# Kernel optimization log

Measured on AMD Instinct MI355X. Metric: run time of the kernel, lower is better.

## Reference

```python
import jax, jax.numpy as jnp
import numpy as np

D = 1024
H = 16
HD = D // H  # 64
LN_EPS = 1e-5


def _layernorm(x, w, b):
    m = jnp.mean(x, axis=-1, keepdims=True)
    v = jnp.mean(jnp.square(x - m), axis=-1, keepdims=True)
    return (x - m) * jax.lax.rsqrt(v + LN_EPS) * w + b


def _attention(x, w_qkv, b_qkv, w_proj, b_proj):
    # x: [B, S, D]. Block-diagonal mask == attention within each sequence,
    # so batched per-sequence attention is exactly equivalent to packed fmha.
    B, S, _ = x.shape
    qkv = x @ w_qkv + b_qkv                      # [B, S, 3D]
    q, k, v = jnp.split(qkv, 3, axis=-1)
    q = q.reshape(B, S, H, HD)
    k = k.reshape(B, S, H, HD)
    v = v.reshape(B, S, H, HD)
    scale = 1.0 / jnp.sqrt(jnp.asarray(HD, dtype=x.dtype))
    scores = jnp.einsum('bqhd,bkhd->bhqk', q, k) * scale  # [B, H, S, S]
    probs = jax.nn.softmax(scores, axis=-1)
    out = jnp.einsum('bhqk,bkhd->bqhd', probs, v).reshape(B, S, D)
    return out @ w_proj + b_proj


def _block(x, w_qkv, b_qkv, w_proj, b_proj, ln1_w, ln1_b,
           w_fc1, b_fc1, w_fc2, b_fc2, ln2_w, ln2_b, gamma1, gamma2):
    # x = x + ls1(attn(norm1(x)))
    x = x + gamma1 * _attention(_layernorm(x, ln1_w, ln1_b), w_qkv, b_qkv, w_proj, b_proj)
    # x = x + ls2(mlp(norm2(x)))
    h = _layernorm(x, ln2_w, ln2_b)
    h = jax.nn.gelu(h @ w_fc1 + b_fc1, approximate=False) @ w_fc2 + b_fc2
    return x + gamma2 * h


def setup_inputs() -> dict:
    key = jax.random.key(0)
    ks = jax.random.split(key, 8)
    s = 0.02
    return {
        'x1': jax.random.normal(ks[0], (8, 1024, D), jnp.float32),
        'x2': jax.random.normal(ks[1], (8, 512, D), jnp.float32),
        'w_qkv': jax.random.normal(ks[2], (D, 3 * D), jnp.float32) * s,
        'b_qkv': jnp.zeros((3 * D,), jnp.float32),
        'w_proj': jax.random.normal(ks[3], (D, D), jnp.float32) * s,
        'b_proj': jnp.zeros((D,), jnp.float32),
        'ln1_w': jnp.ones((D,), jnp.float32),
        'ln1_b': jnp.zeros((D,), jnp.float32),
        'ln2_w': jnp.ones((D,), jnp.float32),
        'ln2_b': jnp.zeros((D,), jnp.float32),
        'w_fc1': jax.random.normal(ks[4], (D, 4 * D), jnp.float32) * s,
        'b_fc1': jnp.zeros((4 * D,), jnp.float32),
        'w_fc2': jax.random.normal(ks[5], (4 * D, D), jnp.float32) * s,
        'b_fc2': jnp.zeros((D,), jnp.float32),
        'gamma1': jnp.full((D,), 1e-5, jnp.float32),  # LayerScale init_values
        'gamma2': jnp.full((D,), 1e-5, jnp.float32),
    }


def reference(x1, x2, w_qkv, b_qkv, w_proj, b_proj, ln1_w, ln1_b,
              ln2_w, ln2_b, w_fc1, b_fc1, w_fc2, b_fc2, gamma1, gamma2):
    params = (w_qkv, b_qkv, w_proj, b_proj, ln1_w, ln1_b,
              w_fc1, b_fc1, w_fc2, b_fc2, ln2_w, ln2_b, gamma1, gamma2)
    y1 = _block(x1, *params)
    y2 = _block(x2, *params)
    return (y1, y2)
```

## Files before the change

kernel.cpp:

```cpp
#include <hip/hip_runtime.h>
#include <cstddef>


typedef __bf16 b16x8 __attribute__((ext_vector_type(8)));
typedef float f32x4 __attribute__((ext_vector_type(4)));
typedef unsigned short u16x8 __attribute__((ext_vector_type(8)));
typedef unsigned short u16x4 __attribute__((ext_vector_type(4)));
typedef float f32x4v __attribute__((ext_vector_type(4)));

__device__ __forceinline__ unsigned short f2bf(float f) {
    unsigned int u = __builtin_bit_cast(unsigned int, f);
    return (unsigned short)((u + 0x7fffu + ((u >> 16) & 1u)) >> 16);
}
__device__ __forceinline__ unsigned short f2bf_trunc(float f) {
    return (unsigned short)(__builtin_bit_cast(unsigned int, f) >> 16);
}

__device__ __forceinline__ float exp2_f(float x) {
#if defined(__has_builtin)
#if __has_builtin(__builtin_amdgcn_exp2f)
    return __builtin_amdgcn_exp2f(x);
#else
    return exp2f(x);
#endif
#else
    return exp2f(x);
#endif
}

#define AS1C(p) ((const __attribute__((address_space(1))) void*)(p))
#define AS3(p)  ((__attribute__((address_space(3))) void*)(p))
#define FENCE() asm volatile("" ::: "memory")

__global__ __launch_bounds__(256) void wtrans_k(const float* __restrict__ in,
                                                unsigned short* __restrict__ out,
                                                int K, int N) {
    __shared__ float tile[32][33];
    int n0 = blockIdx.x << 5, k0 = blockIdx.y << 5;
    int tx = threadIdx.x & 31;
    int ty = threadIdx.x >> 5;
#pragma unroll
    for (int j = 0; j < 4; ++j)
        tile[ty + j * 8][tx] = in[(size_t)(k0 + ty + j * 8) * N + n0 + tx];
    __syncthreads();
#pragma unroll
    for (int j = 0; j < 4; ++j)
        out[(size_t)(n0 + ty + j * 8) * K + k0 + tx] = f2bf(tile[tx][ty + j * 8]);
}

__global__ __launch_bounds__(256) void vtrans_k(const unsigned short* __restrict__ qkv,
                                                unsigned short* __restrict__ vT) {
    __shared__ unsigned short tile[32][40];
    int tok0 = blockIdx.x << 5, c0 = blockIdx.y << 5;
    int tx = threadIdx.x & 31, ty = threadIdx.x >> 5;
#pragma unroll
    for (int j = 0; j < 4; ++j)
        tile[ty + j * 8][tx] = qkv[(size_t)(tok0 + ty + j * 8) * 3072 + 2048 + c0 + tx];
    __syncthreads();
#pragma unroll
    for (int j = 0; j < 4; ++j)
        vT[(size_t)(c0 + ty + j * 8) * 12288 + tok0 + tx] = tile[tx][ty + j * 8];
}

__global__ __launch_bounds__(256) void ln_k(const float* __restrict__ srcA,
                                            const float* __restrict__ srcB, int split,
                                            const float* __restrict__ w,
                                            const float* __restrict__ b,
                                            unsigned short* __restrict__ out) {
    int row = blockIdx.x;
    const float* src = (row < split) ? srcA + (size_t)row * 1024
                                     : srcB + (size_t)(row - split) * 1024;
    int t = threadIdx.x;
    f32x4v v = *(const f32x4v*)(src + t * 4);
    float s = v[0] + v[1] + v[2] + v[3];
    float s2 = v[0] * v[0] + v[1] * v[1] + v[2] * v[2] + v[3] * v[3];
#pragma unroll
    for (int off = 1; off < 64; off <<= 1) {
        s += __shfl_xor(s, off);
        s2 += __shfl_xor(s2, off);
    }
    __shared__ float red[8];
    int wv4 = t >> 6;
    if ((t & 63) == 0) { red[wv4 * 2] = s; red[wv4 * 2 + 1] = s2; }
    __syncthreads();
    s = red[0] + red[2] + red[4] + red[6];
    s2 = red[1] + red[3] + red[5] + red[7];
    float mean = s * (1.0f / 1024.0f);
    float var = s2 * (1.0f / 1024.0f) - mean * mean;
    float rstd = rsqrtf(var + 1e-5f);
    f32x4v wv = *(const f32x4v*)(w + t * 4);
    f32x4v bv = *(const f32x4v*)(b + t * 4);
    u16x4 ov;
#pragma unroll
    for (int j = 0; j < 4; ++j) ov[j] = f2bf((v[j] - mean) * rstd * wv[j] + bv[j]);
    *(u16x4*)(out + (size_t)row * 1024 + t * 4) = ov;
}

template <int BM, int K, int NN, int EPI>
__global__ __launch_bounds__(512, 1) void gemm3_k(
    const unsigned short* __restrict__ A, const unsigned short* __restrict__ BT,
    const float* __restrict__ bias, const float* __restrict__ scale,
    const float* __restrict__ rx1, const float* __restrict__ rx2,
    float* __restrict__ outf, unsigned short* __restrict__ outb) {
    constexpr int NT = K / 64;
    constexpr int ntn = NN >> 8;
    constexpr int GA = BM / 64;
    constexpr int NFR = BM / 32;
    constexpr int HALF = NFR / 2;
    constexpr int ABUF = BM * 128;
    constexpr int STRIDE = ABUF + 32768;
    __shared__ char lds[2 * STRIDE];
    const int t = threadIdx.x;
    const int lane = t & 63, w = t >> 6, lr = lane & 15, lg = lane >> 4;
    const int wm = w >> 2, wn = w & 3;
    const int nwg = gridDim.x;
    const int bid = blockIdx.x;
    const int swz = (bid & 7) * (nwg >> 3) + (bid >> 3);
    const int m0 = (swz / ntn) * BM;
    const int n0 = (swz % ntn) << 8;

    const int srow = t >> 3;
    const int scol = ((t & 7) ^ (srow & 7)) * 8;
    const unsigned short* ga = A + (size_t)(m0 + srow) * K + scol;
    const unsigned short* gb = BT + (size_t)(n0 + srow) * K + scol;

    f32x4 acc[NFR][4] = {};
    b16x8 af[HALF][2], b01[2][2], b23[2][2];

    auto ISSUE_A = [&](int tile, int g) {
        char* dst = lds + (tile & 1) * STRIDE + g * 8192 + t * 16;
        __builtin_amdgcn_global_load_lds(AS1C(ga + (size_t)(g * 64) * K + tile * 64),
                                         AS3(dst), 16, 0, 0);
    };
    auto ISSUE_B = [&](int tile, int g) {
        char* dst = lds + (tile & 1) * STRIDE + ABUF + g * 8192 + t * 16;
        __builtin_amdgcn_global_load_lds(AS1C(gb + (size_t)(g * 64) * K + tile * 64),
                                         AS3(dst), 16, 0, 0);
    };

    const int cs0 = (lg ^ (lr & 7)) * 16;
    const int cs1 = ((4 + lg) ^ (lr & 7)) * 16;

    auto RD_A = [&](const char* buf, int mg) {
#pragma unroll
        for (int mi = 0; mi < HALF; ++mi) {
            const char* p = buf + (wm * (BM / 2) + (mg + mi) * 16 + lr) * 128;
            af[mi][0] = *(const b16x8*)(p + cs0);
            af[mi][1] = *(const b16x8*)(p + cs1);
        }
    };
    auto RD_B = [&](const char* buf, b16x8 (*bf)[2], int ng) {
#pragma unroll
        for (int ni = 0; ni < 2; ++ni) {
            const char* p = buf + ABUF + (wn * 64 + (ng + ni) * 16 + lr) * 128;
            bf[ni][0] = *(const b16x8*)(p + cs0);
            bf[ni][1] = *(const b16x8*)(p + cs1);
        }
    };
    auto MM = [&](int mg, b16x8 (*bf)[2], int ng) {
        __builtin_amdgcn_s_setprio(1);
#pragma unroll
        for (int kk = 0; kk < 2; ++kk)
#pragma unroll
            for (int mi = 0; mi < HALF; ++mi)
#pragma unroll
                for (int ni = 0; ni < 2; ++ni)
                    acc[mg + mi][ng + ni] = __builtin_amdgcn_mfma_f32_16x16x32_bf16(
                        af[mi][kk], bf[ni][kk], acc[mg + mi][ng + ni], 0, 0, 0);
        __builtin_amdgcn_s_setprio(0);
    };
    auto WAIT_GA = [&]() {
        if constexpr (GA == 4) asm volatile("s_waitcnt vmcnt(4)" ::: "memory");
        else                   asm volatile("s_waitcnt vmcnt(3)" ::: "memory");
    };

#pragma unroll
    for (int g = 0; g < GA; ++g) ISSUE_A(0, g);
#pragma unroll
    for (int g = 0; g < 4; ++g) ISSUE_B(0, g);
#pragma unroll
    for (int g = 0; g < GA; ++g) ISSUE_A(1, g);
    WAIT_GA();
    __builtin_amdgcn_s_barrier();
    FENCE();

    for (int kt = 0; kt < NT; ++kt) {
        const char* buf = lds + (kt & 1) * STRIDE;
        RD_A(buf, 0); RD_B(buf, b01, 0);
        if (kt + 1 < NT) { ISSUE_B(kt + 1, 0); ISSUE_B(kt + 1, 1); }
        __builtin_amdgcn_s_barrier(); FENCE();
        MM(0, b01, 0);
        __builtin_amdgcn_s_barrier(); FENCE();
        RD_B(buf, b23, 2);
        if (kt + 1 < NT) { ISSUE_B(kt + 1, 2); ISSUE_B(kt + 1, 3); }
        __builtin_amdgcn_s_barrier(); FENCE();
        MM(0, b23, 2);
        __builtin_amdgcn_s_barrier(); FENCE();
        RD_A(buf, HALF);
        __builtin_amdgcn_s_barrier(); FENCE();
        MM(HALF, b23, 2);
        __builtin_amdgcn_s_barrier(); FENCE();
        if (kt + 2 < NT) {
#pragma unroll
            for (int g = 0; g < GA; ++g) ISSUE_A(kt + 2, g);
        }
        __builtin_amdgcn_s_barrier(); FENCE();
        MM(HALF, b01, 0);
        if (kt + 1 < NT) {
            if (kt + 2 < NT) WAIT_GA();
            else             asm volatile("s_waitcnt vmcnt(0)" ::: "memory");
            __builtin_amdgcn_s_barrier(); FENCE();
        }
    }

    if (EPI == 0 || EPI == 2) {
        __syncthreads();
        char* clb = lds;
        const int rl0 = wm * (BM / 2) + lg * 4;
        const int cl0 = wn * 64 + lr;
#pragma unroll
        for (int n = 0; n < 4; ++n) {
            const int col_l = cl0 + n * 16;
            const float bval = bias[n0 + col_l];
            const int colByte = col_l * 2;
            const int within = colByte & 15;
            const int chunk = colByte >> 4;
#pragma unroll
            for (int m = 0; m < NFR; ++m) {
#pragma unroll
                for (int r = 0; r < 4; ++r) {
                    float c = acc[m][n][r] + bval;
                    if (EPI == 2) {
                        float u = c * (c * c * 0.044715f + 1.0f) * 1.5957691216057308f;
                        c = c * __builtin_amdgcn_rcpf(1.0f + __expf(-u));
                    }
                    const int row_l = rl0 + m * 16 + r;
                    *(unsigned short*)(clb + row_l * 512 +
                                       (((chunk ^ (row_l & 7)) << 4) | within)) = f2bf(c);
                }
            }
        }
        __syncthreads();
#pragma unroll
        for (int it = 0; it < BM / 16; ++it) {
            int idx = it * 512 + t;
            int row = idx >> 5, ch = idx & 31;
            u16x8 v = *(const u16x8*)(clb + row * 512 + ((ch ^ (row & 7)) << 4));
            *(u16x8*)(outb + (size_t)(m0 + row) * NN + n0 + ch * 8) = v;
        }
    } else {
        const int rbase = m0 + wm * (BM / 2) + lg * 4;
        const int cbase = n0 + wn * 64 + lr;
#pragma unroll
        for (int n = 0; n < 4; ++n) {
            int col = cbase + n * 16;
            float bval = bias[col];
            float sval = scale[col];
#pragma unroll
            for (int m = 0; m < NFR; ++m) {
                int row = rbase + m * 16;
#pragma unroll
                for (int r = 0; r < 4; ++r) {
                    float c = acc[m][n][r] + bval;
                    size_t idx = (size_t)(row + r) * NN + col;
                    if (EPI == 1) {
                        float xv = (row + r < 8192) ? rx1[idx] : rx2[idx - (size_t)8192 * 1024];
                        outf[idx] = xv + sval * c;
                    } else {
                        outf[idx] += sval * c;
                    }
                }
            }
        }
    }
}

__global__ __launch_bounds__(512) void attn_k(const unsigned short* __restrict__ qkv,
                                              const unsigned short* __restrict__ vT,
                                              unsigned short* __restrict__ aout) {
    __shared__ char sK[2][8192];
    __shared__ char sV[2][8192];
    __shared__ unsigned short sP[8][16 * 72];
    const int xcd = blockIdx.x & 7;
    const int idx = blockIdx.x >> 3;
    int seq0, S, h, qt;
    if (idx < 128) {
        h = idx & 15; qt = idx >> 4; seq0 = xcd << 10; S = 1024;
    } else {
        int j = idx - 128;
        h = j & 15; qt = j >> 4; seq0 = 8192 + (xcd << 9); S = 512;
    }
    int t = threadIdx.x, lane = t & 63, w = t >> 6, lr = lane & 15, lg = lane >> 4;
    int tok0 = seq0 + qt * 128;
    const size_t hoff = (size_t)h * 64;

    const int srow = t >> 3;
    const int sc = ((t & 7) ^ (srow & 7)) * 8;
    const unsigned short* kg = qkv + (size_t)(seq0 + srow) * 3072 + 1024 + hoff + sc;
    const unsigned short* vg = vT + (size_t)(hoff + srow) * 12288 + seq0 + sc;

    b16x8 aq0, aq1;
    {
        const unsigned short* qb = qkv + (size_t)(tok0 + w * 16 + lr) * 3072 + hoff;
        aq0 = *(const b16x8*)(qb + lg * 8);
        aq1 = *(const b16x8*)(qb + 32 + lg * 8);
    }

    auto STAGE = [&](int kt) {
        int slot = kt & 1;
        __builtin_amdgcn_global_load_lds(AS1C(kg + (size_t)(kt << 6) * 3072),
                                         AS3(sK[slot] + t * 16), 16, 0, 0);
        __builtin_amdgcn_global_load_lds(AS1C(vg + (kt << 6)),
                                         AS3(sV[slot] + t * 16), 16, 0, 0);
    };

    const int swz0 = (lg ^ (lr & 7)) * 16;
    const int swz1 = ((4 + lg) ^ (lr & 7)) * 16;
    const float SC = 0.18033688f;

    float m_run[4] = {-1e30f, -1e30f, -1e30f, -1e30f};
    float l_run[4] = {0.f, 0.f, 0.f, 0.f};
    f32x4 o[4] = {};
    unsigned short* sPw = sP[w];
    const int nkv = S >> 6;

    auto QK = [&](int kt, f32x4 (&s)[4]) {
        const char* kb = sK[kt & 1];
#pragma unroll
        for (int n = 0; n < 4; ++n) {
            const char* kr = kb + (n * 16 + lr) * 128;
            b16x8 bk0 = *(const b16x8*)(kr + swz0);
            b16x8 bk1 = *(const b16x8*)(kr + swz1);
            f32x4 z = {};
            z = __builtin_amdgcn_mfma_f32_16x16x32_bf16(aq0, bk0, z, 0, 0, 0);
            z = __builtin_amdgcn_mfma_f32_16x16x32_bf16(aq1, bk1, z, 0, 0, 0);
            s[n] = z * SC;
        }
    };
    auto SM = [&](f32x4 (&s)[4], b16x8& a0, b16x8& a1) {
        float p[4][4];
#pragma unroll
        for (int r = 0; r < 4; ++r) {
            float tm = fmaxf(fmaxf(s[0][r], s[1][r]), fmaxf(s[2][r], s[3][r]));
            tm = fmaxf(tm, __shfl_xor(tm, 1));
            tm = fmaxf(tm, __shfl_xor(tm, 2));
            tm = fmaxf(tm, __shfl_xor(tm, 4));
            tm = fmaxf(tm, __shfl_xor(tm, 8));
            float mn = fmaxf(m_run[r], tm);
            float alpha = exp2_f(m_run[r] - mn);
            m_run[r] = mn;
            float rs = 0.f;
#pragma unroll
            for (int n = 0; n < 4; ++n) {
                float pv = exp2_f(s[n][r] - mn);
                p[n][r] = pv;
                rs += pv;
            }
            rs += __shfl_xor(rs, 1);
            rs += __shfl_xor(rs, 2);
            rs += __shfl_xor(rs, 4);
            rs += __shfl_xor(rs, 8);
            l_run[r] = l_run[r] * alpha + rs;
#pragma unroll
            for (int n = 0; n < 4; ++n) o[n][r] *= alpha;
        }
#pragma unroll
        for (int r = 0; r < 4; ++r)
#pragma unroll
            for (int n = 0; n < 4; ++n)
                sPw[(lg * 4 + r) * 72 + n * 16 + lr] = f2bf_trunc(p[n][r]);
        a0 = *(const b16x8*)(&sPw[lr * 72 + lg * 8]);
        a1 = *(const b16x8*)(&sPw[lr * 72 + 32 + lg * 8]);
    };

    STAGE(0);
    if (nkv > 1) STAGE(1);
    asm volatile("s_waitcnt vmcnt(0)" ::: "memory");
    __builtin_amdgcn_s_barrier();
    FENCE();
    f32x4 s0[4];
    QK(0, s0);
    b16x8 ap0, ap1;
    SM(s0, ap0, ap1);

    for (int kt = 0; kt < nkv; ++kt) {
        const char* vb = sV[kt & 1];
        b16x8 bv0[4], bv1[4];
#pragma unroll
        for (int n = 0; n < 4; ++n) {
            const char* vr = vb + (n * 16 + lr) * 128;
            bv0[n] = *(const b16x8*)(vr + swz0);
            bv1[n] = *(const b16x8*)(vr + swz1);
        }
        f32x4 s2[4];
        if (kt + 1 < nkv) QK(kt + 1, s2);
        asm volatile("s_waitcnt lgkmcnt(0)" ::: "memory");
        __builtin_amdgcn_s_barrier();
        FENCE();
        if (kt + 2 < nkv) STAGE(kt + 2);
#pragma unroll
        for (int n = 0; n < 4; ++n) {
            o[n] = __builtin_amdgcn_mfma_f32_16x16x32_bf16(ap0, bv0[n], o[n], 0, 0, 0);
            o[n] = __builtin_amdgcn_mfma_f32_16x16x32_bf16(ap1, bv1[n], o[n], 0, 0, 0);
        }
        if (kt + 1 < nkv) {
            SM(s2, ap0, ap1);
            asm volatile("s_waitcnt vmcnt(0)" ::: "memory");
            __builtin_amdgcn_s_barrier();
            FENCE();
        }
    }
    __syncthreads();
    char* ob = sK[0];
#pragma unroll
    for (int r = 0; r < 4; ++r) {
        float inv = __builtin_amdgcn_rcpf(l_run[r]);
        const int row_l = w * 16 + lg * 4 + r;
#pragma unroll
        for (int n = 0; n < 4; ++n) {
            const int colByte = (n * 16 + lr) * 2;
            *(unsigned short*)(ob + row_l * 128 +
                               ((((colByte >> 4) ^ (row_l & 7)) << 4) | (colByte & 15))) =
                f2bf(o[n][r] * inv);
        }
    }
    __syncthreads();
#pragma unroll
    for (int it = 0; it < 2; ++it) {
        int idx2 = it * 512 + t;
        int row = idx2 >> 3, ch = idx2 & 7;
        u16x8 v = *(const u16x8*)(ob + row * 128 + ((ch ^ (row & 7)) << 4));
        *(u16x8*)(aout + (size_t)(tok0 + row) * 1024 + hoff + ch * 8) = v;
    }
}

extern "C" void kernel_launch(void* const* d_in, const int* in_sizes, int n_in,
                              void* d_out, int out_size, void* d_ws, size_t ws_size,
                              hipStream_t stream) {
    const float* x1     = (const float*)d_in[0];
    const float* x2     = (const float*)d_in[1];
    const float* w_qkv  = (const float*)d_in[2];
    const float* b_qkv  = (const float*)d_in[3];
    const float* w_proj = (const float*)d_in[4];
    const float* b_proj = (const float*)d_in[5];
    const float* ln1w   = (const float*)d_in[6];
    const float* ln1b   = (const float*)d_in[7];
    const float* ln2w   = (const float*)d_in[8];
    const float* ln2b   = (const float*)d_in[9];
    const float* w_fc1  = (const float*)d_in[10];
    const float* b_fc1  = (const float*)d_in[11];
    const float* w_fc2  = (const float*)d_in[12];
    const float* b_fc2  = (const float*)d_in[13];
    const float* gamma1 = (const float*)d_in[14];
    const float* gamma2 = (const float*)d_in[15];
    float* out = (float*)d_out;
    char* ws = (char*)d_ws;

    unsigned short* wqkvT  = (unsigned short*)(ws);
    unsigned short* wprojT = (unsigned short*)(ws + 6291456);
    unsigned short* wfc1T  = (unsigned short*)(ws + 8388608);
    unsigned short* wfc2T  = (unsigned short*)(ws + 16777216);
    unsigned short* lnbuf  = (unsigned short*)(ws + 25165824);
    unsigned short* qkvbuf = (unsigned short*)(ws + 50331648);
    unsigned short* attnbuf= (unsigned short*)(ws + 125829120);
    unsigned short* actbuf = (unsigned short*)(ws + 50331648);
    unsigned short* vTbuf  = lnbuf;

    wtrans_k<<<dim3(96, 32), 256, 0, stream>>>(w_qkv, wqkvT, 1024, 3072);
    wtrans_k<<<dim3(32, 32), 256, 0, stream>>>(w_proj, wprojT, 1024, 1024);
    wtrans_k<<<dim3(128, 32), 256, 0, stream>>>(w_fc1, wfc1T, 1024, 4096);
    wtrans_k<<<dim3(32, 128), 256, 0, stream>>>(w_fc2, wfc2T, 4096, 1024);
    ln_k<<<12288, 256, 0, stream>>>(x1, x2, 8192, ln1w, ln1b, lnbuf);
    gemm3_k<192, 1024, 3072, 0><<<768, 512, 0, stream>>>(lnbuf, wqkvT, b_qkv, nullptr,
                                                         nullptr, nullptr, nullptr, qkvbuf);
    vtrans_k<<<dim3(384, 32), 256, 0, stream>>>(qkvbuf, vTbuf);
    attn_k<<<1536, 512, 0, stream>>>(qkvbuf, vTbuf, attnbuf);
    gemm3_k<192, 1024, 1024, 1><<<256, 512, 0, stream>>>(attnbuf, wprojT, b_proj, gamma1,
                                                         x1, x2, out, nullptr);
    ln_k<<<12288, 256, 0, stream>>>(out, out + (size_t)8192 * 1024, 8192, ln2w, ln2b, lnbuf);
    gemm3_k<256, 1024, 4096, 2><<<768, 512, 0, stream>>>(lnbuf, wfc1T, b_fc1, nullptr,
                                                         nullptr, nullptr, nullptr, actbuf);
    gemm3_k<192, 4096, 1024, 3><<<256, 512, 0, stream>>>(actbuf, wfc2T, b_fc2, gamma2,
                                                         nullptr, nullptr, out, nullptr);
}
```

Before: 554.8 us.

## Run QKV, FC1 and FC2 GEMMs in FP8 with scaled MFMA

Converts weights (scaled by 16) and layernorm outputs to FP8 E4M3, and adds a new gemm4_k kernel that uses the 16x16x128 scaled FP8 MFMA for the QKV, FC1 and FC2 projections. The GELU epilogue writes FP8 activations for FC2. This halves operand bytes and doubles the matrix-core rate compared with bf16, in exchange for reduced numerical precision that may threaten tolerance. The projection GEMM stays bf16.

```diff
diff --git a/kernel.cpp b/kernel.cpp
--- a/kernel.cpp
+++ b/kernel.cpp
@@ -7,6 +7,8 @@
 typedef unsigned short u16x8 __attribute__((ext_vector_type(8)));
 typedef unsigned short u16x4 __attribute__((ext_vector_type(4)));
 typedef float f32x4v __attribute__((ext_vector_type(4)));
+typedef int i32x4v __attribute__((ext_vector_type(4)));
+typedef int i32x8v __attribute__((ext_vector_type(8)));
 
 __device__ __forceinline__ unsigned short f2bf(float f) {
     unsigned int u = __builtin_bit_cast(unsigned int, f);
@@ -14,6 +16,25 @@
 }
 __device__ __forceinline__ unsigned short f2bf_trunc(float f) {
     return (unsigned short)(__builtin_bit_cast(unsigned int, f) >> 16);
+}
+
+__device__ __forceinline__ unsigned char f2fp8(float x) {
+    unsigned int u = __builtin_bit_cast(unsigned int, x);
+    unsigned char s = (unsigned char)((u >> 24) & 0x80u);
+    unsigned int au = u & 0x7FFFFFFFu;
+    float a = __builtin_bit_cast(float, au);
+    if (a >= 448.0f) return s | 0x7E;
+    if (a < 0.015625f) {
+        int m = (int)(a * 512.0f + 0.5f);
+        if (m >= 8) return s | 0x08;
+        return s | (unsigned char)m;
+    }
+    unsigned int ur = au + 0x7FFFFu + ((au >> 20) & 1u);
+    int e = (int)((ur >> 23) & 0xFFu) - 127;
+    if (e > 8) return s | 0x7E;
+    unsigned int m3 = (ur >> 20) & 7u;
+    if (e == 8 && m3 > 6) return s | 0x7E;
+    return s | (unsigned char)(((e + 7) << 3) | m3);
 }
 
 __device__ __forceinline__ float exp2_f(float x) {
@@ -32,8 +53,9 @@
 #define AS3(p)  ((__attribute__((address_space(3))) void*)(p))
 #define FENCE() asm volatile("" ::: "memory")
 
+template <bool FP8>
 __global__ __launch_bounds__(256) void wtrans_k(const float* __restrict__ in,
-                                                unsigned short* __restrict__ out,
+                                                void* __restrict__ outv,
                                                 int K, int N) {
     __shared__ float tile[32][33];
     int n0 = blockIdx.x << 5, k0 = blockIdx.y << 5;
@@ -44,8 +66,14 @@
         tile[ty + j * 8][tx] = in[(size_t)(k0 + ty + j * 8) * N + n0 + tx];
     __syncthreads();
 #pragma unroll
-    for (int j = 0; j < 4; ++j)
-        out[(size_t)(n0 + ty + j * 8) * K + k0 + tx] = f2bf(tile[tx][ty + j * 8]);
+    for (int j = 0; j < 4; ++j) {
+        if (FP8)
+            ((unsigned char*)outv)[(size_t)(n0 + ty + j * 8) * K + k0 + tx] =
+                f2fp8(tile[tx][ty + j * 8] * 16.0f);
+        else
+            ((unsigned short*)outv)[(size_t)(n0 + ty + j * 8) * K + k0 + tx] =
+                f2bf(tile[tx][ty + j * 8]);
+    }
 }
 
 __global__ __launch_bounds__(256) void vtrans_k(const unsigned short* __restrict__ qkv,
@@ -66,7 +94,7 @@
                                             const float* __restrict__ srcB, int split,
                                             const float* __restrict__ w,
                                             const float* __restrict__ b,
-                                            unsigned short* __restrict__ out) {
+                                            unsigned char* __restrict__ out) {
     int row = blockIdx.x;
     const float* src = (row < split) ? srcA + (size_t)row * 1024
                                      : srcB + (size_t)(row - split) * 1024;
@@ -90,18 +118,221 @@
     float rstd = rsqrtf(var + 1e-5f);
     f32x4v wv = *(const f32x4v*)(w + t * 4);
     f32x4v bv = *(const f32x4v*)(b + t * 4);
-    u16x4 ov;
-#pragma unroll
-    for (int j = 0; j < 4; ++j) ov[j] = f2bf((v[j] - mean) * rstd * wv[j] + bv[j]);
-    *(u16x4*)(out + (size_t)row * 1024 + t * 4) = ov;
+    unsigned int pk = 0;
+#pragma unroll
+    for (int j = 0; j < 4; ++j)
+        pk |= (unsigned int)f2fp8((v[j] - mean) * rstd * wv[j] + bv[j]) << (8 * j);
+    *(unsigned int*)(out + (size_t)row * 1024 + t * 4) = pk;
 }
 
 template <int BM, int K, int NN, int EPI>
+__global__ __launch_bounds__(512, 1) void gemm4_k(
+    const unsigned char* __restrict__ A, const unsigned char* __restrict__ BT,
+    const float* __restrict__ bias, const float* __restrict__ scale,
+    float* __restrict__ outf, unsigned short* __restrict__ outb,
+    unsigned char* __restrict__ outc) {
+    constexpr int NT = K / 128;
+    constexpr int ntn = NN >> 8;
+    constexpr int GA = BM / 64;
+    constexpr int NFR = BM / 32;
+    constexpr int HALF = NFR / 2;
+    constexpr int ABUF = BM * 128;
+    constexpr int STRIDE = ABUF + 32768;
+    __shared__ char lds[2 * STRIDE];
+    const int t = threadIdx.x;
+    const int lane = t & 63, w = t >> 6, lr = lane & 15, lg = lane >> 4;
+    const int wm = w >> 2, wn = w & 3;
+    const int nwg = gridDim.x;
+    const int bid = blockIdx.x;
+    const int swz = (bid & 7) * (nwg >> 3) + (bid >> 3);
+    const int m0 = (swz / ntn) * BM;
+    const int n0 = (swz % ntn) << 8;
+
+    const int srow = t >> 3;
+    const int scol = ((t & 7) ^ (srow & 7)) * 16;
+    const unsigned char* ga = A + (size_t)(m0 + srow) * K + scol;
+    const unsigned char* gb = BT + (size_t)(n0 + srow) * K + scol;
+
+    f32x4 acc[NFR][4] = {};
+    i32x8v af[HALF], b01[2], b23[2];
+
+    auto ISSUE_A = [&](int tile, int g) {
+        char* dst = lds + (tile & 1) * STRIDE + g * 8192 + t * 16;
+        __builtin_amdgcn_global_load_lds(AS1C(ga + (size_t)(g * 64) * K + tile * 128),
+                                         AS3(dst), 16, 0, 0);
+    };
+    auto ISSUE_B = [&](int tile, int g) {
+        char* dst = lds + (tile & 1) * STRIDE + ABUF + g * 8192 + t * 16;
+        __builtin_amdgcn_global_load_lds(AS1C(gb + (size_t)(g * 64) * K + tile * 128),
+                                         AS3(dst), 16, 0, 0);
+    };
+
+    const int cs0 = ((2 * lg) ^ (lr & 7)) * 16;
+    const int cs1 = ((2 * lg + 1) ^ (lr & 7)) * 16;
+
+    auto LD32 = [&](const char* p) -> i32x8v {
+        i32x4v lo = *(const i32x4v*)(p + cs0);
+        i32x4v hi = *(const i32x4v*)(p + cs1);
+        i32x8v r;
+        r[0] = lo[0]; r[1] = lo[1]; r[2] = lo[2]; r[3] = lo[3];
+        r[4] = hi[0]; r[5] = hi[1]; r[6] = hi[2]; r[7] = hi[3];
+        return r;
+    };
+    auto RD_A = [&](const char* buf, int mg) {
+#pragma unroll
+        for (int mi = 0; mi < HALF; ++mi)
+            af[mi] = LD32(buf + (wm * (BM / 2) + (mg + mi) * 16 + lr) * 128);
+    };
+    auto RD_B = [&](const char* buf, i32x8v* bf, int ng) {
+#pragma unroll
+        for (int ni = 0; ni < 2; ++ni)
+            bf[ni] = LD32(buf + ABUF + (wn * 64 + (ng + ni) * 16 + lr) * 128);
+    };
+    auto MM = [&](int mg, i32x8v* bf, int ng) {
+        __builtin_amdgcn_s_setprio(1);
+#pragma unroll
+        for (int mi = 0; mi < HALF; ++mi)
+#pragma unroll
+            for (int ni = 0; ni < 2; ++ni)
+                acc[mg + mi][ng + ni] = __builtin_amdgcn_mfma_scale_f32_16x16x128_f8f6f4(
+                    af[mi], bf[ni], acc[mg + mi][ng + ni],
+                    0, 0, 0, 0x7F7F7F7F, 0, 0x7B7B7B7B);
+        __builtin_amdgcn_s_setprio(0);
+    };
+    auto WAIT_GA = [&]() {
+        if constexpr (GA == 4) asm volatile("s_waitcnt vmcnt(4)" ::: "memory");
+        else                   asm volatile("s_waitcnt vmcnt(3)" ::: "memory");
+    };
+
+#pragma unroll
+    for (int g = 0; g < GA; ++g) ISSUE_A(0, g);
+#pragma unroll
+    for (int g = 0; g < 4; ++g) ISSUE_B(0, g);
+#pragma unroll
+    for (int g = 0; g < GA; ++g) ISSUE_A(1, g);
+    WAIT_GA();
+    __builtin_amdgcn_s_barrier();
+    FENCE();
+
+    for (int kt = 0; kt < NT; ++kt) {
+        const char* buf = lds + (kt & 1) * STRIDE;
+        RD_A(buf, 0); RD_B(buf, b01, 0);
+        if (kt + 1 < NT) { ISSUE_B(kt + 1, 0); ISSUE_B(kt + 1, 1); }
+        __builtin_amdgcn_s_barrier(); FENCE();
+        MM(0, b01, 0);
+        __builtin_amdgcn_s_barrier(); FENCE();
+        RD_B(buf, b23, 2);
+        if (kt + 1 < NT) { ISSUE_B(kt + 1, 2); ISSUE_B(kt + 1, 3); }
+        __builtin_amdgcn_s_barrier(); FENCE();
+        MM(0, b23, 2);
+        __builtin_amdgcn_s_barrier(); FENCE();
+        RD_A(buf, HALF);
+        __builtin_amdgcn_s_barrier(); FENCE();
+        MM(HALF, b23, 2);
+        __builtin_amdgcn_s_barrier(); FENCE();
+        if (kt + 2 < NT) {
+#pragma unroll
+            for (int g = 0; g < GA; ++g) ISSUE_A(kt + 2, g);
+        }
+        __builtin_amdgcn_s_barrier(); FENCE();
+        MM(HALF, b01, 0);
+        if (kt + 1 < NT) {
+            if (kt + 2 < NT) WAIT_GA();
+            else             asm volatile("s_waitcnt vmcnt(0)" ::: "memory");
+            __builtin_amdgcn_s_barrier(); FENCE();
+        }
+    }
+
+    if (EPI == 0) {
+        __syncthreads();
+        char* clb = lds;
+        const int rl0 = wm * (BM / 2) + lg * 4;
+        const int cl0 = wn * 64 + lr;
+#pragma unroll
+        for (int n = 0; n < 4; ++n) {
+            const int col_l = cl0 + n * 16;
+            const float bval = bias[n0 + col_l];
+            const int colByte = col_l * 2;
+            const int within = colByte & 15;
+            const int chunk = colByte >> 4;
+#pragma unroll
+            for (int m = 0; m < NFR; ++m) {
+#pragma unroll
+                for (int r = 0; r < 4; ++r) {
+                    const int row_l = rl0 + m * 16 + r;
+                    *(unsigned short*)(clb + row_l * 512 +
+                                       (((chunk ^ (row_l & 7)) << 4) | within)) =
+                        f2bf(acc[m][n][r] + bval);
+                }
+            }
+        }
+        __syncthreads();
+#pragma unroll
+        for (int it = 0; it < BM / 16; ++it) {
+            int idx = it * 512 + t;
+            int row = idx >> 5, ch = idx & 31;
+            u16x8 v = *(const u16x8*)(clb + row * 512 + ((ch ^ (row & 7)) << 4));
+            *(u16x8*)(outb + (size_t)(m0 + row) * NN + n0 + ch * 8) = v;
+        }
+    } else if (EPI == 2) {
+        __syncthreads();
+        char* clb = lds;
+        const int rl0 = wm * (BM / 2) + lg * 4;
+        const int cl0 = wn * 64 + lr;
+#pragma unroll
+        for (int n = 0; n < 4; ++n) {
+            const int col_l = cl0 + n * 16;
+            const float bval = bias[n0 + col_l];
+            const int within = col_l & 15;
+            const int chunk = col_l >> 4;
+#pragma unroll
+            for (int m = 0; m < NFR; ++m) {
+#pragma unroll
+                for (int r = 0; r < 4; ++r) {
+                    float c = acc[m][n][r] + bval;
+                    float u = c * (c * c * 0.044715f + 1.0f) * 1.5957691216057308f;
+                    c = c * __builtin_amdgcn_rcpf(1.0f + __expf(-u));
+                    const int row_l = rl0 + m * 16 + r;
+                    *(unsigned char*)(clb + row_l * 256 +
+                                      (((chunk ^ (row_l & 7)) << 4) | within)) = f2fp8(c);
+                }
+            }
+        }
+        __syncthreads();
+#pragma unroll
+        for (int it = 0; it < BM / 32; ++it) {
+            int idx = it * 512 + t;
+            int row = idx >> 4, ch = idx & 15;
+            i32x4v v = *(const i32x4v*)(clb + row * 256 + ((ch ^ (row & 7)) << 4));
+            *(i32x4v*)(outc + (size_t)(m0 + row) * NN + n0 + ch * 16) = v;
+        }
+    } else {
+        const int rbase = m0 + wm * (BM / 2) + lg * 4;
+        const int cbase = n0 + wn * 64 + lr;
+#pragma unroll
+        for (int n = 0; n < 4; ++n) {
+            int col = cbase + n * 16;
+            float bval = bias[col];
+            float sval = scale[col];
+#pragma unroll
+            for (int m = 0; m < NFR; ++m) {
+                int row = rbase + m * 16;
+#pragma unroll
+                for (int r = 0; r < 4; ++r) {
+                    size_t idx = (size_t)(row + r) * NN + col;
+                    outf[idx] += sval * (acc[m][n][r] + bval);
+                }
+            }
+        }
+    }
+}
+
+template <int BM, int K, int NN>
 __global__ __launch_bounds__(512, 1) void gemm3_k(
     const unsigned short* __restrict__ A, const unsigned short* __restrict__ BT,
     const float* __restrict__ bias, const float* __restrict__ scale,
     const float* __restrict__ rx1, const float* __restrict__ rx2,
-    float* __restrict__ outf, unsigned short* __restrict__ outb) {
+    float* __restrict__ outf) {
     constexpr int NT = K / 64;
     constexpr int ntn = NN >> 8;
     constexpr int GA = BM / 64;
@@ -213,63 +444,22 @@
         }
     }
 
-    if (EPI == 0 || EPI == 2) {
-        __syncthreads();
-        char* clb = lds;
-        const int rl0 = wm * (BM / 2) + lg * 4;
-        const int cl0 = wn * 64 + lr;
-#pragma unroll
-        for (int n = 0; n < 4; ++n) {
-            const int col_l = cl0 + n * 16;
-            const float bval = bias[n0 + col_l];
-            const int colByte = col_l * 2;
-            const int within = colByte & 15;
-            const int chunk = colByte >> 4;
-#pragma unroll
-            for (int m = 0; m < NFR; ++m) {
-#pragma unroll
-                for (int r = 0; r < 4; ++r) {
-                    float c = acc[m][n][r] + bval;
-                    if (EPI == 2) {
-                        float u = c * (c * c * 0.044715f + 1.0f) * 1.5957691216057308f;
-                        c = c * __builtin_amdgcn_rcpf(1.0f + __expf(-u));
-                    }
-                    const int row_l = rl0 + m * 16 + r;
-                    *(unsigned short*)(clb + row_l * 512 +
-                                       (((chunk ^ (row_l & 7)) << 4) | within)) = f2bf(c);
-                }
-            }
-        }
-        __syncthreads();
-#pragma unroll
-        for (int it = 0; it < BM / 16; ++it) {
-            int idx = it * 512 + t;
-            int row = idx >> 5, ch = idx & 31;
-            u16x8 v = *(const u16x8*)(clb + row * 512 + ((ch ^ (row & 7)) << 4));
-            *(u16x8*)(outb + (size_t)(m0 + row) * NN + n0 + ch * 8) = v;
-        }
-    } else {
-        const int rbase = m0 + wm * (BM / 2) + lg * 4;
-        const int cbase = n0 + wn * 64 + lr;
-#pragma unroll
-        for (int n = 0; n < 4; ++n) {
-            int col = cbase + n * 16;
-            float bval = bias[col];
-            float sval = scale[col];
-#pragma unroll
-            for (int m = 0; m < NFR; ++m) {
-                int row = rbase + m * 16;
-#pragma unroll
-                for (int r = 0; r < 4; ++r) {
-                    float c = acc[m][n][r] + bval;
-                    size_t idx = (size_t)(row + r) * NN + col;
-                    if (EPI == 1) {
-                        float xv = (row + r < 8192) ? rx1[idx] : rx2[idx - (size_t)8192 * 1024];
-                        outf[idx] = xv + sval * c;
-                    } else {
-                        outf[idx] += sval * c;
-                    }
-                }
+    const int rbase = m0 + wm * (BM / 2) + lg * 4;
+    const int cbase = n0 + wn * 64 + lr;
+#pragma unroll
+    for (int n = 0; n < 4; ++n) {
+        int col = cbase + n * 16;
+        float bval = bias[col];
+        float sval = scale[col];
+#pragma unroll
+        for (int m = 0; m < NFR; ++m) {
+            int row = rbase + m * 16;
+#pragma unroll
+            for (int r = 0; r < 4; ++r) {
+                float c = acc[m][n][r] + bval;
+                size_t idx = (size_t)(row + r) * NN + col;
+                float xv = (row + r < 8192) ? rx1[idx] : rx2[idx - (size_t)8192 * 1024];
+                outf[idx] = xv + sval * c;
             }
         }
     }
@@ -456,30 +646,30 @@
     float* out = (float*)d_out;
     char* ws = (char*)d_ws;
 
-    unsigned short* wqkvT  = (unsigned short*)(ws);
+    unsigned char*  wqkvT  = (unsigned char*)(ws);
     unsigned short* wprojT = (unsigned short*)(ws + 6291456);
-    unsigned short* wfc1T  = (unsigned short*)(ws + 8388608);
-    unsigned short* wfc2T  = (unsigned short*)(ws + 16777216);
-    unsigned short* lnbuf  = (unsigned short*)(ws + 25165824);
+    unsigned char*  wfc1T  = (unsigned char*)(ws + 8388608);
+    unsigned char*  wfc2T  = (unsigned char*)(ws + 16777216);
+    unsigned char*  lnbuf  = (unsigned char*)(ws + 25165824);
     unsigned short* qkvbuf = (unsigned short*)(ws + 50331648);
     unsigned short* attnbuf= (unsigned short*)(ws + 125829120);
-    unsigned short* actbuf = (unsigned short*)(ws + 50331648);
-    unsigned short* vTbuf  = lnbuf;
-
-    wtrans_k<<<dim3(96, 32), 256, 0, stream>>>(w_qkv, wqkvT, 1024, 3072);
-    wtrans_k<<<dim3(32, 32), 256, 0, stream>>>(w_proj, wprojT, 1024, 1024);
-    wtrans_k<<<dim3(128, 32), 256, 0, stream>>>(w_fc1, wfc1T, 1024, 4096);
-    wtrans_k<<<dim3(32, 128), 256, 0, stream>>>(w_fc2, wfc2T, 4096, 1024);
+    unsigned char*  actbuf = (unsigned char*)(ws + 50331648);
+    unsigned short* vTbuf  = (unsigned short*)(ws + 25165824);
+
+    wtrans_k<true ><<<dim3(96, 32), 256, 0, stream>>>(w_qkv, wqkvT, 1024, 3072);
+    wtrans_k<false><<<dim3(32, 32), 256, 0, stream>>>(w_proj, wprojT, 1024, 1024);
+    wtrans_k<true ><<<dim3(128, 32), 256, 0, stream>>>(w_fc1, wfc1T, 1024, 4096);
+    wtrans_k<true ><<<dim3(32, 128), 256, 0, stream>>>(w_fc2, wfc2T, 4096, 1024);
     ln_k<<<12288, 256, 0, stream>>>(x1, x2, 8192, ln1w, ln1b, lnbuf);
-    gemm3_k<192, 1024, 3072, 0><<<768, 512, 0, stream>>>(lnbuf, wqkvT, b_qkv, nullptr,
-                                                         nullptr, nullptr, nullptr, qkvbuf);
+    gemm4_k<192, 1024, 3072, 0><<<768, 512, 0, stream>>>(lnbuf, wqkvT, b_qkv, nullptr,
+                                                         nullptr, qkvbuf, nullptr);
     vtrans_k<<<dim3(384, 32), 256, 0, stream>>>(qkvbuf, vTbuf);
     attn_k<<<1536, 512, 0, stream>>>(qkvbuf, vTbuf, attnbuf);
-    gemm3_k<192, 1024, 1024, 1><<<256, 512, 0, stream>>>(attnbuf, wprojT, b_proj, gamma1,
-                                                         x1, x2, out, nullptr);
+    gemm3_k<192, 1024, 1024><<<256, 512, 0, stream>>>(attnbuf, wprojT, b_proj, gamma1,
+                                                      x1, x2, out);
     ln_k<<<12288, 256, 0, stream>>>(out, out + (size_t)8192 * 1024, 8192, ln2w, ln2b, lnbuf);
-    gemm3_k<256, 1024, 4096, 2><<<768, 512, 0, stream>>>(lnbuf, wfc1T, b_fc1, nullptr,
-                                                         nullptr, nullptr, nullptr, actbuf);
-    gemm3_k<192, 4096, 1024, 3><<<256, 512, 0, stream>>>(actbuf, wfc2T, b_fc2, gamma2,
-                                                         nullptr, nullptr, out, nullptr);
-}
+    gemm4_k<256, 1024, 4096, 2><<<768, 512, 0, stream>>>(lnbuf, wfc1T, b_fc1, nullptr,
+                                                         nullptr, nullptr, actbuf);
+    gemm4_k<192, 4096, 1024, 3><<<256, 512, 0, stream>>>(actbuf, wfc2T, b_fc2, gamma2,
+                                                         out, nullptr, nullptr);
+}
```

Measured after the change: 1.254 ms. +126.1%, slower.
